# Kernel tuning notes

Measured on AMD Instinct MI355X. Metric: run time of the kernel, lower is better.

Reference implementation:

```python
import jax, jax.numpy as jnp
import numpy as np


def _quant_dequant_rowwise(v):
    # vector-wise absmax int8 quantization along the last axis, then dequant.
    # Exactly reproduces dequantized result of the int8 GEMM operand:
    # Cx = round(v/s) clipped to [-127,127]; dq = Cx * s.
    s = jnp.max(jnp.abs(v), axis=-1, keepdims=True) / 127.0
    s = jnp.maximum(s, 1e-8)
    q = jnp.clip(jnp.round(v / s), -127.0, 127.0)
    return q * s


def setup_inputs() -> dict:
    key = jax.random.key(0)
    k1, k2, k3 = jax.random.split(key, 3)
    B, S, K, N = 4, 2048, 4096, 4096
    x = jax.random.normal(k1, (B, S, K), dtype=jnp.float32)
    # amplify a few feature columns so |col| exceeds the 6.0 outlier threshold,
    # exercising the LLM.int8() mixed-precision decomposition path
    x = x.at[..., ::256].multiply(10.0)
    W = jax.random.normal(k2, (N, K), dtype=jnp.float32) * 0.02
    bias = jax.random.normal(k3, (N,), dtype=jnp.float32) * 0.01
    return {"x": x, "W": W, "bias": bias, "threshold": 6}


def reference(x, W, bias, threshold):
    # LLM.int8() matmul with outlier decomposition (bnb.matmul semantics):
    #  1. columns of x whose absmax > threshold are outliers -> fp16/fp32 path
    #  2. remaining x columns + full W are vector-wise int8 quantized, int8 GEMM,
    #     dequant with per-row scales (exactly equal to dq(x) @ dq(W).T)
    #  3. out = int8-part + x_outlier @ W_outlier.T + bias
    thr = jnp.asarray(threshold, dtype=x.dtype)
    B_shape = x.shape[:-1]
    K = x.shape[-1]
    x2 = x.reshape(-1, K)                                   # [M, K]
    colmax = jnp.max(jnp.abs(x2), axis=0)                   # [K]
    out_mask = (colmax > thr).astype(x.dtype)               # 1.0 on outlier cols
    x_int = x2 * (1.0 - out_mask)                           # zero outlier cols
    dq_x = _quant_dequant_rowwise(x_int)                    # [M, K]
    dq_w = _quant_dequant_rowwise(W)                        # [N, K]
    out = dq_x @ dq_w.T                                     # int8 GEMM, dequantized
    out = out + (x2 * out_mask) @ (W * out_mask).T          # fp outlier GEMM
    out = out + bias
    return out.reshape(*B_shape, W.shape[0])
```

## Files before the change

kernel.cpp:

```cpp
#include <hip/hip_runtime.h>

typedef unsigned short u16;
typedef unsigned char u8;
typedef unsigned int u32;
typedef __attribute__((ext_vector_type(4))) float f32x4;
typedef __attribute__((ext_vector_type(16))) float f32x16;
typedef __attribute__((ext_vector_type(8))) __bf16 bf16x8;
typedef __attribute__((ext_vector_type(4))) int i32x4;
typedef __attribute__((ext_vector_type(16))) int i32x16;

__device__ __forceinline__ u16 f2bf(float f) {
  u32 u = __float_as_uint(f);
  u32 r = (u + 0x7fffu + ((u >> 16) & 1u)) >> 16;
  return (u16)r;
}

__device__ __forceinline__ float load_thr(const int* p) {
  int iv = *p;
  float fv = __int_as_float(iv);
  if (fv >= 1.0f && fv <= 1.0e6f) return fv;
  return (float)iv;
}

__device__ __forceinline__ void gload_lds16(const void* g, void* l) {
  __builtin_amdgcn_global_load_lds(
      (const __attribute__((address_space(1))) void*)g,
      (__attribute__((address_space(3))) void*)l, 16, 0, 0);
}

__global__ void k_init_cm(u32* cm, int K) {
  int i = blockIdx.x * 256 + threadIdx.x;
  if (i < K) cm[i] = 0u;
}

__global__ __launch_bounds__(256) void k_colmax(const float* __restrict__ x,
                                                u32* __restrict__ cm, int M,
                                                int K, int rpb) {
  int c4 = blockIdx.x * 256 + threadIdx.x;
  int r0 = blockIdx.y * rpb;
  int r1 = r0 + rpb;
  if (r1 > M) r1 = M;
  f32x4 mx = {0.f, 0.f, 0.f, 0.f};
  for (int r = r0; r < r1; ++r) {
    f32x4 v = *(const f32x4*)&x[(size_t)r * K + (size_t)c4 * 4];
#pragma unroll
    for (int i = 0; i < 4; ++i) mx[i] = fmaxf(mx[i], fabsf(v[i]));
  }
#pragma unroll
  for (int i = 0; i < 4; ++i)
    atomicMax(&cm[c4 * 4 + i], __float_as_uint(mx[i]));
}

__global__ void k_ocols(const u32* __restrict__ cm, const int* __restrict__ thr_i,
                        int K, int* __restrict__ meta) {
  int lane = threadIdx.x;
  float thr = load_thr(thr_i);
  const float* cmf = (const float*)cm;
  int per = K >> 6;
  int base = lane * per;
  int c = 0;
  for (int i = 0; i < per; ++i) c += (cmf[base + i] > thr) ? 1 : 0;
  int inc = c;
  for (int off = 1; off < 64; off <<= 1) {
    int t = __shfl_up(inc, off);
    if (lane >= off) inc += t;
  }
  int excl = inc - c;
  int total = __shfl(inc, 63);
  if (lane == 0) meta[0] = total < 64 ? total : 64;
  int idx = excl;
  for (int i = 0; i < per; ++i) {
    if (cmf[base + i] > thr) {
      if (idx < 64) meta[1 + idx] = base + i;
      idx++;
    }
  }
  for (int j = total + lane; j < 64; j += 64) meta[1 + j] = -1;
}

__global__ __launch_bounds__(256) void k_quant8(
    const float* __restrict__ src, const u32* __restrict__ cm,
    const int* __restrict__ thr_i, const int* __restrict__ meta,
    char* __restrict__ qdst, float* __restrict__ sdst, u16* __restrict__ odst,
    int K, int zero_outlier) {
  int row = blockIdx.x;
  int tid = threadIdx.x;
  float thr = load_thr(thr_i);
  const float* sr = src + (size_t)row * K;
  const float* cmf = (const float*)cm;

  float v[16];
  u32 omask = 0;
  float lmax = 0.f;
#pragma unroll
  for (int j = 0; j < 4; ++j) {
    int c4 = j * 256 + tid;
    f32x4 val = *(const f32x4*)&sr[c4 * 4];
    f32x4 cv = *(const f32x4*)&cmf[c4 * 4];
#pragma unroll
    for (int i = 0; i < 4; ++i) {
      float xv = val[i];
      v[j * 4 + i] = xv;
      bool is_out = cv[i] > thr;
      if (is_out) omask |= 1u << (j * 4 + i);
      if (!is_out || !zero_outlier) lmax = fmaxf(lmax, fabsf(xv));
    }
  }
  float m = lmax;
#pragma unroll
  for (int off = 32; off >= 1; off >>= 1) m = fmaxf(m, __shfl_down(m, off));
  __shared__ float red[4];
  int lane = tid & 63, wv = tid >> 6;
  if (lane == 0) red[wv] = m;
  __syncthreads();
  float rm = fmaxf(fmaxf(red[0], red[1]), fmaxf(red[2], red[3]));
  float s = fmaxf(rm / 127.0f, 1e-8f);

  u32* q32 = (u32*)(qdst + (size_t)row * K);
#pragma unroll
  for (int j = 0; j < 4; ++j) {
    int c4 = j * 256 + tid;
    u32 pk = 0;
#pragma unroll
    for (int i = 0; i < 4; ++i) {
      float xv = v[j * 4 + i];
      int iq;
      if (zero_outlier && (omask & (1u << (j * 4 + i)))) {
        iq = 0;
      } else {
        float q = rintf(xv / s);
        q = fminf(fmaxf(q, -127.f), 127.f);
        iq = (int)q;
      }
      pk |= ((u32)(u8)(char)iq) << (8 * i);
    }
    q32[c4] = pk;
  }
  if (tid == 0) sdst[row] = s;
  if (tid < 64) {
    int n_out = meta[0];
    int oc = meta[1 + tid];
    u16 ov = 0;
    if (tid < n_out && oc >= 0) ov = f2bf(sr[oc]);
    odst[(size_t)row * 64 + tid] = ov;
  }
}

__global__ __launch_bounds__(512, 2) void k_gemm_i8(
    const char* __restrict__ qx, const char* __restrict__ qw,
    const float* __restrict__ sx, const float* __restrict__ sw,
    const float* __restrict__ bias, const char* __restrict__ xo,
    const char* __restrict__ wo, float* __restrict__ out, int M, int N,
    int K) {
  extern __shared__ char lds_raw[];
  int tid = threadIdx.x;
  int lane = tid & 63, wave = tid >> 6;
  int wm = wave >> 2, wn = wave & 3;

  int nwg = gridDim.x;
  int bid = blockIdx.x;
  int swzb = (bid & 7) * (nwg >> 3) + (bid >> 3);
  int nbn = N / 256;
  int bm = swzb / nbn, bn = swzb % nbn;
  int r0 = bm * 256, c0 = bn * 256;

  int g0 = tid, g1 = 512 + tid;
  int row0s = g0 >> 3, col0b = ((g0 & 7) ^ (row0s & 7)) << 4;
  int row1s = g1 >> 3, col1b = ((g1 & 7) ^ (row1s & 7)) << 4;

#define AH(buf, h) (lds_raw + (buf) * 65536 + (h) * 16384)
#define BHALF(buf, h) (lds_raw + (buf) * 65536 + 32768 + (h) * 16384)

#define STAGE(dstb, srcb, rowbase, kb)                                        \
  {                                                                           \
    gload_lds16((srcb) + (size_t)((rowbase) + row0s) * K + (kb) + col0b,      \
                (dstb) + g0 * 16);                                            \
    gload_lds16((srcb) + (size_t)((rowbase) + row1s) * K + (kb) + col1b,      \
                (dstb) + g1 * 16);                                            \
  }

#define LDAI(dst, buf, q, ks)                                                 \
  {                                                                           \
    int rl = (q) * 32 + (lane & 31);                                          \
    dst = *(const i32x4*)(AH(buf, wm) + rl * 128 +                            \
                          ((((ks) * 2 + (lane >> 5)) ^ (rl & 7)) << 4));      \
  }
#define LDBI(dst, buf, nf, ks)                                                \
  {                                                                           \
    int rl = ((wn & 1) << 6) + (nf) * 32 + (lane & 31);                       \
    dst = *(const i32x4*)(BHALF(buf, wn >> 1) + rl * 128 +                    \
                          ((((ks) * 2 + (lane >> 5)) ^ (rl & 7)) << 4));      \
  }

#define MFI(q, nf, av, bv)                                                    \
  asm volatile("v_mfma_i32_32x32x32_i8 %0, %1, %2, %0"                        \
               : "+v"(acc[q][nf])                                             \
               : "v"(av), "v"(bv))

#define PHASEI(buf, q, PREF, TAILWAIT)                                        \
  {                                                                           \
    if ((q) == 0) {                                                           \
      LDBI(Bfi[0], buf, 0, 0); LDBI(Bfi[1], buf, 0, 1);                       \
      LDBI(Bfi[2], buf, 0, 2); LDBI(Bfi[3], buf, 0, 3);                       \
      LDBI(Bfi[4], buf, 1, 0); LDBI(Bfi[5], buf, 1, 1);                       \
      LDBI(Bfi[6], buf, 1, 2); LDBI(Bfi[7], buf, 1, 3);                       \
    }                                                                         \
    i32x4 a0, a1, a2, a3;                                                     \
    LDAI(a0, buf, q, 0);                                                      \
    LDAI(a1, buf, q, 1);                                                      \
    LDAI(a2, buf, q, 2);                                                      \
    LDAI(a3, buf, q, 3);                                                      \
    PREF;                                                                     \
    if ((q) == 0) asm volatile("s_waitcnt lgkmcnt(8)" ::: "memory");          \
    __builtin_amdgcn_s_barrier();                                             \
    asm volatile("s_waitcnt lgkmcnt(0)" ::: "memory");                        \
    __builtin_amdgcn_s_setprio(1);                                            \
    MFI(q, 0, a0, Bfi[0]);                                                    \
    MFI(q, 0, a1, Bfi[1]);                                                    \
    MFI(q, 0, a2, Bfi[2]);                                                    \
    MFI(q, 0, a3, Bfi[3]);                                                    \
    MFI(q, 1, a0, Bfi[4]);                                                    \
    MFI(q, 1, a1, Bfi[5]);                                                    \
    MFI(q, 1, a2, Bfi[6]);                                                    \
    MFI(q, 1, a3, Bfi[7]);                                                    \
    __builtin_amdgcn_s_setprio(0);                                            \
    TAILWAIT;                                                                 \
    __builtin_amdgcn_s_barrier();                                             \
  }

#define WV4 asm volatile("s_waitcnt vmcnt(4)" ::: "memory")

  i32x16 acc[4][2] = {};
  i32x4 Bfi[8];

  STAGE(AH(0, 0), qx, r0, 0);
  STAGE(AH(0, 1), qx, r0 + 128, 0);
  STAGE(BHALF(0, 0), qw, c0, 0);
  STAGE(BHALF(0, 1), qw, c0 + 128, 0);
  STAGE(BHALF(1, 0), qw, c0, 128);
  STAGE(BHALF(1, 1), qw, c0 + 128, 128);
  WV4;
  __builtin_amdgcn_s_barrier();

  int nit = K / 256;
  for (int it = 0; it < nit; ++it) {
    int kt1 = it * 256 + 128;
    int kb2 = it * 256 + 256;
    kb2 = (kb2 < K) ? kb2 : 0;
    int kb3 = it * 256 + 384;
    kb3 = (kb3 < K) ? kb3 : 0;
    PHASEI(0, 0, STAGE(AH(1, 0), qx, r0, kt1), );
    PHASEI(0, 1, STAGE(AH(1, 1), qx, r0 + 128, kt1), );
    PHASEI(0, 2, STAGE(BHALF(0, 0), qw, c0, kb2), );
    PHASEI(0, 3, STAGE(BHALF(0, 1), qw, c0 + 128, kb2), WV4);
    PHASEI(1, 0, STAGE(AH(0, 0), qx, r0, kb2), );
    PHASEI(1, 1, STAGE(AH(0, 1), qx, r0 + 128, kb2), );
    PHASEI(1, 2, STAGE(BHALF(1, 0), qw, c0, kb3), );
    PHASEI(1, 3, STAGE(BHALF(1, 1), qw, c0 + 128, kb3), WV4);
  }

#pragma unroll
  for (int i = 0; i < 4; ++i) {
    int g = tid + i * 512;
    int rw = g >> 3;
    int cb = ((g & 7) ^ (rw & 7)) << 4;
    gload_lds16(xo + (size_t)(r0 + rw) * 128 + cb, lds_raw + g * 16);
  }
#pragma unroll
  for (int i = 0; i < 4; ++i) {
    int g = tid + i * 512;
    int rw = g >> 3;
    int cb = ((g & 7) ^ (rw & 7)) << 4;
    gload_lds16(wo + (size_t)(c0 + rw) * 128 + cb, lds_raw + 32768 + g * 16);
  }

  f32x16 facc[4][2];
  float swv0 = sw[c0 + wn * 64 + (lane & 31)];
  float swv1 = sw[c0 + wn * 64 + 32 + (lane & 31)];
#pragma unroll
  for (int fm = 0; fm < 4; ++fm) {
    int gmb = r0 + wm * 128 + fm * 32 + 4 * (lane >> 5);
    f32x4 s4a = *(const f32x4*)&sx[gmb];
    f32x4 s4b = *(const f32x4*)&sx[gmb + 8];
    f32x4 s4c = *(const f32x4*)&sx[gmb + 16];
    f32x4 s4d = *(const f32x4*)&sx[gmb + 24];
#pragma unroll
    for (int reg = 0; reg < 16; ++reg) {
      float sxv = (reg < 4) ? s4a[reg & 3]
                : (reg < 8) ? s4b[reg & 3]
                : (reg < 12) ? s4c[reg & 3] : s4d[reg & 3];
      facc[fm][0][reg] = (float)acc[fm][0][reg] * sxv * swv0;
      facc[fm][1][reg] = (float)acc[fm][1][reg] * sxv * swv1;
    }
  }

  asm volatile("s_waitcnt vmcnt(0)" ::: "memory");
  __builtin_amdgcn_s_barrier();

#pragma unroll
  for (int ks = 0; ks < 4; ++ks) {
    int rn0 = wn * 64 + (lane & 31);
    int rn1 = rn0 + 32;
    bf16x8 ob0 = *(const bf16x8*)(lds_raw + 32768 + rn0 * 128 +
                                  (((ks * 2 + (lane >> 5)) ^ (rn0 & 7)) << 4));
    bf16x8 ob1 = *(const bf16x8*)(lds_raw + 32768 + rn1 * 128 +
                                  (((ks * 2 + (lane >> 5)) ^ (rn1 & 7)) << 4));
#pragma unroll
    for (int fm = 0; fm < 4; ++fm) {
      int rl = wm * 128 + fm * 32 + (lane & 31);
      bf16x8 oa = *(const bf16x8*)(lds_raw + rl * 128 +
                                   (((ks * 2 + (lane >> 5)) ^ (rl & 7)) << 4));
      facc[fm][0] = __builtin_amdgcn_mfma_f32_32x32x16_bf16(oa, ob0,
                                                            facc[fm][0], 0, 0, 0);
      facc[fm][1] = __builtin_amdgcn_mfma_f32_32x32x16_bf16(oa, ob1,
                                                            facc[fm][1], 0, 0, 0);
    }
  }

  float bv0 = bias[c0 + wn * 64 + (lane & 31)];
  float bv1 = bias[c0 + wn * 64 + 32 + (lane & 31)];
  int gc0 = c0 + wn * 64 + (lane & 31);
#pragma unroll
  for (int fm = 0; fm < 4; ++fm) {
#pragma unroll
    for (int reg = 0; reg < 16; ++reg) {
      int gm = r0 + wm * 128 + fm * 32 + (reg & 3) + 8 * (reg >> 2) +
               4 * (lane >> 5);
      float* orow = out + (size_t)gm * N + gc0;
      orow[0] = facc[fm][0][reg] + bv0;
      orow[32] = facc[fm][1][reg] + bv1;
    }
  }
}

extern "C" void kernel_launch(void* const* d_in, const int* in_sizes, int n_in,
                              void* d_out, int out_size, void* d_ws,
                              size_t ws_size, hipStream_t stream) {
  const float* x = (const float*)d_in[0];
  const float* W = (const float*)d_in[1];
  const float* bias = (const float*)d_in[2];
  const int* thr = (const int*)d_in[3];
  float* out = (float*)d_out;

  int N = in_sizes[2];
  int K = in_sizes[1] / N;
  int M = in_sizes[0] / K;

  char* ws = (char*)d_ws;
  u32* cm = (u32*)ws;
  int* meta = (int*)(ws + 16384);
  float* sx = (float*)(ws + 32768);
  float* sw = (float*)(ws + 32768 + (size_t)M * 4);
  char* xo = ws + 32768 + (size_t)(M + N) * 4;
  char* wo = xo + (size_t)M * 128;
  char* qx = wo + (size_t)N * 128;
  char* qw = qx + (size_t)M * K;

  k_init_cm<<<dim3((K + 255) / 256), dim3(256), 0, stream>>>(cm, K);

  {
    int gx = K / 1024;
    int gy = 128;
    int rpb = (M + gy - 1) / gy;
    k_colmax<<<dim3(gx, gy), dim3(256), 0, stream>>>(x, cm, M, K, rpb);
  }

  k_ocols<<<dim3(1), dim3(64), 0, stream>>>(cm, thr, K, meta);

  k_quant8<<<dim3(M), dim3(256), 0, stream>>>(x, cm, thr, meta, qx, sx,
                                              (u16*)xo, K, 1);
  k_quant8<<<dim3(N), dim3(256), 0, stream>>>(W, cm, thr, meta, qw, sw,
                                              (u16*)wo, K, 0);

  (void)hipFuncSetAttribute((const void*)k_gemm_i8,
                            hipFuncAttributeMaxDynamicSharedMemorySize,
                            131072);
  int nwg = (M / 256) * (N / 256);
  k_gemm_i8<<<dim3(nwg), dim3(512), 131072, stream>>>(qx, qw, sx, sw, bias,
                                                      xo, wo, out, M, N, K);
}
```

Measured before the change: 253.1 us.

## Pre-tile int8 operands into MFMA fragment layout, stream A from global directly

```diff
diff --git a/kernel.cpp b/kernel.cpp
--- a/kernel.cpp
+++ b/kernel.cpp
@@ -116,7 +116,8 @@
   float rm = fmaxf(fmaxf(red[0], red[1]), fmaxf(red[2], red[3]));
   float s = fmaxf(rm / 127.0f, 1e-8f);
 
-  u32* q32 = (u32*)(qdst + (size_t)row * K);
+  u32* qt = (u32*)qdst;
+  size_t rowpart = (size_t)(row >> 5) * (K >> 5) * 256 + (size_t)(row & 31) * 8;
 #pragma unroll
   for (int j = 0; j < 4; ++j) {
     int c4 = j * 256 + tid;
@@ -134,7 +135,7 @@
       }
       pk |= ((u32)(u8)(char)iq) << (8 * i);
     }
-    q32[c4] = pk;
+    qt[rowpart + (size_t)(c4 >> 3) * 256 + (c4 & 7)] = pk;
   }
   if (tid == 0) sdst[row] = s;
   if (tid < 64) {
@@ -155,108 +156,102 @@
   extern __shared__ char lds_raw[];
   int tid = threadIdx.x;
   int lane = tid & 63, wave = tid >> 6;
-  int wm = wave >> 2, wn = wave & 3;
-
-  int nwg = gridDim.x;
-  int bid = blockIdx.x;
+  int wm = wave >> 1, wn = wave & 1;
+
+  int nwg = gridDim.x, bid = blockIdx.x;
   int swzb = (bid & 7) * (nwg >> 3) + (bid >> 3);
-  int nbn = N / 256;
+  int nbn = N >> 8;
   int bm = swzb / nbn, bn = swzb % nbn;
-  int r0 = bm * 256, c0 = bn * 256;
-
-  int g0 = tid, g1 = 512 + tid;
-  int row0s = g0 >> 3, col0b = ((g0 & 7) ^ (row0s & 7)) << 4;
-  int row1s = g1 >> 3, col1b = ((g1 & 7) ^ (row1s & 7)) << 4;
-
-#define AH(buf, h) (lds_raw + (buf) * 65536 + (h) * 16384)
-#define BHALF(buf, h) (lds_raw + (buf) * 65536 + 32768 + (h) * 16384)
-
-#define STAGE(dstb, srcb, rowbase, kb)                                        \
+  int r0 = bm << 8, c0 = bn << 8;
+  int K32 = K >> 5;
+  int lbyte = (lane & 31) * 32 + (lane >> 5) * 16;
+
+  size_t bpart[4];
+  int bg[4];
+#pragma unroll
+  for (int i = 0; i < 4; ++i) {
+    int g = tid + i * 512;
+    int b = g >> 6;
+    int nb = b >> 2, kb = b & 3;
+    bpart[i] = ((size_t)((c0 >> 5) + nb) * K32 + kb) * 1024 + (g & 63) * 16;
+    bg[i] = g;
+  }
+#define STAGE_B(bufp, kt)                                                     \
   {                                                                           \
-    gload_lds16((srcb) + (size_t)((rowbase) + row0s) * K + (kb) + col0b,      \
-                (dstb) + g0 * 16);                                            \
-    gload_lds16((srcb) + (size_t)((rowbase) + row1s) * K + (kb) + col1b,      \
-                (dstb) + g1 * 16);                                            \
-  }
-
-#define LDAI(dst, buf, q, ks)                                                 \
+    _Pragma("unroll") for (int i = 0; i < 4; ++i)                             \
+        gload_lds16(qw + bpart[i] + ((size_t)((kt) >> 5) << 10),              \
+                    (bufp) + bg[i] * 16);                                     \
+  }
+
+  const char* abase0 = qx + ((size_t)((r0 >> 5) + wm * 2) * K32 << 10) + lbyte;
+  const char* abase1 = abase0 + ((size_t)K32 << 10);
+#define LOAD_A(ar, kt)                                                        \
   {                                                                           \
-    int rl = (q) * 32 + (lane & 31);                                          \
-    dst = *(const i32x4*)(AH(buf, wm) + rl * 128 +                            \
-                          ((((ks) * 2 + (lane >> 5)) ^ (rl & 7)) << 4));      \
-  }
-#define LDBI(dst, buf, nf, ks)                                                \
-  {                                                                           \
-    int rl = ((wn & 1) << 6) + (nf) * 32 + (lane & 31);                       \
-    dst = *(const i32x4*)(BHALF(buf, wn >> 1) + rl * 128 +                    \
-                          ((((ks) * 2 + (lane >> 5)) ^ (rl & 7)) << 4));      \
-  }
+    _Pragma("unroll") for (int ks = 0; ks < 4; ++ks) {                        \
+      ar[ks] = *(const i32x4*)(abase0 + ((size_t)(((kt) >> 5) + ks) << 10));  \
+      ar[4 + ks] =                                                            \
+          *(const i32x4*)(abase1 + ((size_t)(((kt) >> 5) + ks) << 10));       \
+    }                                                                         \
+  }
+
+#define BFR(dst, bufp, nf, ks)                                                \
+  dst = *(const i32x4*)((bufp) + ((((wn * 4 + (nf)) * 4 + (ks)) << 10)) +     \
+                        lbyte);
 
 #define MFI(q, nf, av, bv)                                                    \
   asm volatile("v_mfma_i32_32x32x32_i8 %0, %1, %2, %0"                        \
                : "+v"(acc[q][nf])                                             \
                : "v"(av), "v"(bv))
 
-#define PHASEI(buf, q, PREF, TAILWAIT)                                        \
+#define CLUST(ac, p)                                                          \
   {                                                                           \
-    if ((q) == 0) {                                                           \
-      LDBI(Bfi[0], buf, 0, 0); LDBI(Bfi[1], buf, 0, 1);                       \
-      LDBI(Bfi[2], buf, 0, 2); LDBI(Bfi[3], buf, 0, 3);                       \
-      LDBI(Bfi[4], buf, 1, 0); LDBI(Bfi[5], buf, 1, 1);                       \
-      LDBI(Bfi[6], buf, 1, 2); LDBI(Bfi[7], buf, 1, 3);                       \
+    __builtin_amdgcn_s_setprio(1);                                            \
+    _Pragma("unroll") for (int ks = 0; ks < 4; ++ks) {                        \
+      MFI(0, 2 * (p), ac[ks], Bf[ks]);                                        \
+      MFI(0, 2 * (p) + 1, ac[ks], Bf[4 + ks]);                                \
+      MFI(1, 2 * (p), ac[4 + ks], Bf[ks]);                                    \
+      MFI(1, 2 * (p) + 1, ac[4 + ks], Bf[4 + ks]);                            \
     }                                                                         \
-    i32x4 a0, a1, a2, a3;                                                     \
-    LDAI(a0, buf, q, 0);                                                      \
-    LDAI(a1, buf, q, 1);                                                      \
-    LDAI(a2, buf, q, 2);                                                      \
-    LDAI(a3, buf, q, 3);                                                      \
-    PREF;                                                                     \
-    if ((q) == 0) asm volatile("s_waitcnt lgkmcnt(8)" ::: "memory");          \
+    __builtin_amdgcn_s_setprio(0);                                            \
+  }
+
+#define TILE(bufc, bufn, ac, an, ktn)                                         \
+  {                                                                           \
+    STAGE_B(bufn, ktn);                                                       \
+    LOAD_A(an, ktn);                                                          \
+    __builtin_amdgcn_sched_barrier(0);                                        \
+    i32x4 Bf[8];                                                              \
+    BFR(Bf[0], bufc, 0, 0); BFR(Bf[1], bufc, 0, 1);                           \
+    BFR(Bf[2], bufc, 0, 2); BFR(Bf[3], bufc, 0, 3);                           \
+    BFR(Bf[4], bufc, 1, 0); BFR(Bf[5], bufc, 1, 1);                           \
+    BFR(Bf[6], bufc, 1, 2); BFR(Bf[7], bufc, 1, 3);                           \
+    CLUST(ac, 0);                                                             \
+    BFR(Bf[0], bufc, 2, 0); BFR(Bf[1], bufc, 2, 1);                           \
+    BFR(Bf[2], bufc, 2, 2); BFR(Bf[3], bufc, 2, 3);                           \
+    BFR(Bf[4], bufc, 3, 0); BFR(Bf[5], bufc, 3, 1);                           \
+    BFR(Bf[6], bufc, 3, 2); BFR(Bf[7], bufc, 3, 3);                           \
+    CLUST(ac, 1);                                                             \
+    asm volatile("s_waitcnt vmcnt(0)" ::: "memory");                          \
     __builtin_amdgcn_s_barrier();                                             \
-    asm volatile("s_waitcnt lgkmcnt(0)" ::: "memory");                        \
-    __builtin_amdgcn_s_setprio(1);                                            \
-    MFI(q, 0, a0, Bfi[0]);                                                    \
-    MFI(q, 0, a1, Bfi[1]);                                                    \
-    MFI(q, 0, a2, Bfi[2]);                                                    \
-    MFI(q, 0, a3, Bfi[3]);                                                    \
-    MFI(q, 1, a0, Bfi[4]);                                                    \
-    MFI(q, 1, a1, Bfi[5]);                                                    \
-    MFI(q, 1, a2, Bfi[6]);                                                    \
-    MFI(q, 1, a3, Bfi[7]);                                                    \
-    __builtin_amdgcn_s_setprio(0);                                            \
-    TAILWAIT;                                                                 \
-    __builtin_amdgcn_s_barrier();                                             \
-  }
-
-#define WV4 asm volatile("s_waitcnt vmcnt(4)" ::: "memory")
-
-  i32x16 acc[4][2] = {};
-  i32x4 Bfi[8];
-
-  STAGE(AH(0, 0), qx, r0, 0);
-  STAGE(AH(0, 1), qx, r0 + 128, 0);
-  STAGE(BHALF(0, 0), qw, c0, 0);
-  STAGE(BHALF(0, 1), qw, c0 + 128, 0);
-  STAGE(BHALF(1, 0), qw, c0, 128);
-  STAGE(BHALF(1, 1), qw, c0 + 128, 128);
-  WV4;
+  }
+
+  char* buf0 = lds_raw;
+  char* buf1 = lds_raw + 32768;
+  i32x16 acc[2][4] = {};
+  i32x4 aA[8], aB[8];
+
+  STAGE_B(buf0, 0);
+  LOAD_A(aA, 0);
+  asm volatile("s_waitcnt vmcnt(0)" ::: "memory");
   __builtin_amdgcn_s_barrier();
 
   int nit = K / 256;
   for (int it = 0; it < nit; ++it) {
     int kt1 = it * 256 + 128;
-    int kb2 = it * 256 + 256;
-    kb2 = (kb2 < K) ? kb2 : 0;
-    int kb3 = it * 256 + 384;
-    kb3 = (kb3 < K) ? kb3 : 0;
-    PHASEI(0, 0, STAGE(AH(1, 0), qx, r0, kt1), );
-    PHASEI(0, 1, STAGE(AH(1, 1), qx, r0 + 128, kt1), );
-    PHASEI(0, 2, STAGE(BHALF(0, 0), qw, c0, kb2), );
-    PHASEI(0, 3, STAGE(BHALF(0, 1), qw, c0 + 128, kb2), WV4);
-    PHASEI(1, 0, STAGE(AH(0, 0), qx, r0, kb2), );
-    PHASEI(1, 1, STAGE(AH(0, 1), qx, r0 + 128, kb2), );
-    PHASEI(1, 2, STAGE(BHALF(1, 0), qw, c0, kb3), );
-    PHASEI(1, 3, STAGE(BHALF(1, 1), qw, c0 + 128, kb3), WV4);
+    int kt2 = it * 256 + 256;
+    kt2 = (kt2 < K) ? kt2 : 0;
+    TILE(buf0, buf1, aA, aB, kt1);
+    TILE(buf1, buf0, aB, aA, kt2);
   }
 
 #pragma unroll
@@ -265,21 +260,19 @@
     int rw = g >> 3;
     int cb = ((g & 7) ^ (rw & 7)) << 4;
     gload_lds16(xo + (size_t)(r0 + rw) * 128 + cb, lds_raw + g * 16);
-  }
-#pragma unroll
-  for (int i = 0; i < 4; ++i) {
-    int g = tid + i * 512;
-    int rw = g >> 3;
-    int cb = ((g & 7) ^ (rw & 7)) << 4;
     gload_lds16(wo + (size_t)(c0 + rw) * 128 + cb, lds_raw + 32768 + g * 16);
   }
 
-  f32x16 facc[4][2];
-  float swv0 = sw[c0 + wn * 64 + (lane & 31)];
-  float swv1 = sw[c0 + wn * 64 + 32 + (lane & 31)];
-#pragma unroll
-  for (int fm = 0; fm < 4; ++fm) {
-    int gmb = r0 + wm * 128 + fm * 32 + 4 * (lane >> 5);
+  f32x16 facc[2][4];
+  float swv[4], bv[4];
+#pragma unroll
+  for (int nf = 0; nf < 4; ++nf) {
+    swv[nf] = sw[c0 + wn * 128 + nf * 32 + (lane & 31)];
+    bv[nf] = bias[c0 + wn * 128 + nf * 32 + (lane & 31)];
+  }
+#pragma unroll
+  for (int q = 0; q < 2; ++q) {
+    int gmb = r0 + wm * 64 + q * 32 + 4 * (lane >> 5);
     f32x4 s4a = *(const f32x4*)&sx[gmb];
     f32x4 s4b = *(const f32x4*)&sx[gmb + 8];
     f32x4 s4c = *(const f32x4*)&sx[gmb + 16];
@@ -289,8 +282,9 @@
       float sxv = (reg < 4) ? s4a[reg & 3]
                 : (reg < 8) ? s4b[reg & 3]
                 : (reg < 12) ? s4c[reg & 3] : s4d[reg & 3];
-      facc[fm][0][reg] = (float)acc[fm][0][reg] * sxv * swv0;
-      facc[fm][1][reg] = (float)acc[fm][1][reg] * sxv * swv1;
+#pragma unroll
+      for (int nf = 0; nf < 4; ++nf)
+        facc[q][nf][reg] = (float)acc[q][nf][reg] * sxv * swv[nf];
     }
   }
 
@@ -299,36 +293,35 @@
 
 #pragma unroll
   for (int ks = 0; ks < 4; ++ks) {
-    int rn0 = wn * 64 + (lane & 31);
-    int rn1 = rn0 + 32;
-    bf16x8 ob0 = *(const bf16x8*)(lds_raw + 32768 + rn0 * 128 +
-                                  (((ks * 2 + (lane >> 5)) ^ (rn0 & 7)) << 4));
-    bf16x8 ob1 = *(const bf16x8*)(lds_raw + 32768 + rn1 * 128 +
-                                  (((ks * 2 + (lane >> 5)) ^ (rn1 & 7)) << 4));
-#pragma unroll
-    for (int fm = 0; fm < 4; ++fm) {
-      int rl = wm * 128 + fm * 32 + (lane & 31);
+    bf16x8 ob[4];
+#pragma unroll
+    for (int nf = 0; nf < 4; ++nf) {
+      int rn = wn * 128 + nf * 32 + (lane & 31);
+      ob[nf] = *(const bf16x8*)(lds_raw + 32768 + rn * 128 +
+                                (((ks * 2 + (lane >> 5)) ^ (rn & 7)) << 4));
+    }
+#pragma unroll
+    for (int q = 0; q < 2; ++q) {
+      int rl = wm * 64 + q * 32 + (lane & 31);
       bf16x8 oa = *(const bf16x8*)(lds_raw + rl * 128 +
                                    (((ks * 2 + (lane >> 5)) ^ (rl & 7)) << 4));
-      facc[fm][0] = __builtin_amdgcn_mfma_f32_32x32x16_bf16(oa, ob0,
-                                                            facc[fm][0], 0, 0, 0);
-      facc[fm][1] = __builtin_amdgcn_mfma_f32_32x32x16_bf16(oa, ob1,
-                                                            facc[fm][1], 0, 0, 0);
-    }
-  }
-
-  float bv0 = bias[c0 + wn * 64 + (lane & 31)];
-  float bv1 = bias[c0 + wn * 64 + 32 + (lane & 31)];
-  int gc0 = c0 + wn * 64 + (lane & 31);
-#pragma unroll
-  for (int fm = 0; fm < 4; ++fm) {
+#pragma unroll
+      for (int nf = 0; nf < 4; ++nf)
+        facc[q][nf] = __builtin_amdgcn_mfma_f32_32x32x16_bf16(
+            oa, ob[nf], facc[q][nf], 0, 0, 0);
+    }
+  }
+
+#pragma unroll
+  for (int q = 0; q < 2; ++q) {
 #pragma unroll
     for (int reg = 0; reg < 16; ++reg) {
-      int gm = r0 + wm * 128 + fm * 32 + (reg & 3) + 8 * (reg >> 2) +
+      int gm = r0 + wm * 64 + q * 32 + (reg & 3) + 8 * (reg >> 2) +
                4 * (lane >> 5);
-      float* orow = out + (size_t)gm * N + gc0;
-      orow[0] = facc[fm][0][reg] + bv0;
-      orow[32] = facc[fm][1][reg] + bv1;
+      float* orow = out + (size_t)gm * N + c0 + wn * 128 + (lane & 31);
+#pragma unroll
+      for (int nf = 0; nf < 4; ++nf)
+        orow[nf * 32] = facc[q][nf][reg] + bv[nf];
     }
   }
 }
@@ -374,8 +367,8 @@
 
   (void)hipFuncSetAttribute((const void*)k_gemm_i8,
                             hipFuncAttributeMaxDynamicSharedMemorySize,
-                            131072);
+                            65536);
   int nwg = (M / 256) * (N / 256);
-  k_gemm_i8<<<dim3(nwg), dim3(512), 131072, stream>>>(qx, qw, sx, sw, bias,
-                                                      xo, wo, out, M, N, K);
-}
+  k_gemm_i8<<<dim3(nwg), dim3(512), 65536, stream>>>(qx, qw, sx, sw, bias,
+                                                     xo, wo, out, M, N, K);
+}
```

Result: slower. 266.6 us (+5.4%).
